# Optimization experiments

Measured on AMD Instinct MI355X. Metric: run time of the kernel, lower is better.

The kernel has to match this reference:

```python
import math
import jax, jax.numpy as jnp
import numpy as np

B, T, H = 4096, 49, 512

def setup_inputs() -> dict:
    key = jax.random.key(0)
    ks = jax.random.split(key, 13)
    sc = 1.0 / math.sqrt(H)
    return {
        "v": jax.random.normal(ks[0], (B, T, H), dtype=jnp.float32),
        "h": jax.random.normal(ks[1], (B, H), dtype=jnp.float32),
        "s": jax.random.normal(ks[2], (B, H), dtype=jnp.float32),
        "W_h": jax.random.normal(ks[3], (H, H), dtype=jnp.float32) * sc,
        "b_h": jax.random.normal(ks[4], (H,), dtype=jnp.float32) * sc,
        "W_v": jax.random.normal(ks[5], (H, H), dtype=jnp.float32) * sc,
        "b_v": jax.random.normal(ks[6], (H,), dtype=jnp.float32) * sc,
        "w_z": jax.random.normal(ks[7], (H,), dtype=jnp.float32) * sc,
        "b_z": jax.random.normal(ks[8], (), dtype=jnp.float32) * sc,
        "W_s": jax.random.normal(ks[9], (H, H), dtype=jnp.float32) * sc,
        "b_s": jax.random.normal(ks[10], (H,), dtype=jnp.float32) * sc,
        "w_beta": jax.random.normal(ks[11], (H,), dtype=jnp.float32) * sc,
        "b_beta": jax.random.normal(ks[12], (), dtype=jnp.float32) * sc,
    }

def reference(v, h, s, W_h, b_h, W_v, b_v, w_z, b_z, W_s, b_s, w_beta, b_beta):
    # eval mode: dropout is identity
    h_proj = h @ W_h + b_h                                  # [B, H]
    v_proj = jnp.einsum('bth,hk->btk', v, W_v) + b_v        # [B, T, H]
    z = jnp.tanh(h_proj[:, None, :] + v_proj)               # [B, T, H]
    z = jnp.einsum('bth,h->bt', z, w_z) + b_z               # [B, T]
    beta = jnp.tanh((s @ W_s + b_s + h_proj) * math.sqrt(0.5))  # [B, H]
    beta = (beta @ w_beta + b_beta)[:, None]                # [B, 1]
    a = jax.nn.softmax(jnp.concatenate([z, beta], axis=1), axis=1)  # [B, T+1]
    v_ext = jnp.concatenate([v, s[:, None, :]], axis=1)     # [B, T+1, H]
    c = jnp.einsum('bt,bth->bh', a, v_ext)                  # [B, H]
    return c
```

## Files before the change

kernel.cpp:

```cpp
#include <hip/hip_runtime.h>
#include <stdint.h>

#define B_ 4096
#define T_ 49
#define H_ 512
#define BT_ (B_*T_)
#define BB 16

typedef __bf16 bf16x8 __attribute__((ext_vector_type(8)));
typedef float  f32x4  __attribute__((ext_vector_type(4)));
typedef unsigned short ushort_;

__device__ __forceinline__ ushort_ f2bf(float f){
  unsigned int u = __float_as_uint(f);
  u += 0x7fffu + ((u >> 16) & 1u);
  return (ushort_)(u >> 16);
}

__device__ __forceinline__ float fast_tanh(float x){
  float e = __expf(2.0f * x);
  return 1.0f - 2.0f * __builtin_amdgcn_rcpf(e + 1.0f);
}

__global__ __launch_bounds__(256) void k_pack(const float* __restrict__ W,
                                              ushort_* __restrict__ pack){
  int idx = blockIdx.x * 256 + threadIdx.x;
  int lane = idx & 63;
  int gt   = (idx >> 6) & 31;
  int kk   = idx >> 11;
  int col  = gt*16 + (lane & 15);
  int k0   = kk*32 + (lane >> 4)*8;
  ushort4 lo, hi;
  lo.x = f2bf(W[(k0+0)*H_ + col]);
  lo.y = f2bf(W[(k0+1)*H_ + col]);
  lo.z = f2bf(W[(k0+2)*H_ + col]);
  lo.w = f2bf(W[(k0+3)*H_ + col]);
  hi.x = f2bf(W[(k0+4)*H_ + col]);
  hi.y = f2bf(W[(k0+5)*H_ + col]);
  hi.z = f2bf(W[(k0+6)*H_ + col]);
  hi.w = f2bf(W[(k0+7)*H_ + col]);
  ushort4* dst = (ushort4*)pack;
  dst[idx*2]   = lo;
  dst[idx*2+1] = hi;
}

__global__ __launch_bounds__(256) void k_proj2(
    const float* __restrict__ h, const float* __restrict__ s,
    const ushort_* __restrict__ whp, const ushort_* __restrict__ wsp,
    const float* __restrict__ bh, const float* __restrict__ bs,
    const float* __restrict__ bv, const float* __restrict__ wbeta,
    const float* __restrict__ bbeta_p,
    float* __restrict__ hpb, float* __restrict__ beta)
{
  __shared__ __align__(16) ushort_ hl[16*H_];
  __shared__ __align__(16) ushort_ sl[16*H_];
  __shared__ float zwp[4][16];
  const int tid = threadIdx.x;
  const int w = tid >> 6, lane = tid & 63;
  const int l15 = lane & 15, l4 = lane >> 4;
  const int b0 = blockIdx.x * 16;

  {
    const int r = tid >> 4;
    const float4* hsrc = (const float4*)(h + (size_t)(b0+r)*H_);
    const float4* ssrc = (const float4*)(s + (size_t)(b0+r)*H_);
    #pragma unroll
    for(int p=0;p<8;p++){
      int q  = (tid & 15) + p*16;
      int k0 = q*4;
      float4 fh = hsrc[q];
      float4 fs = ssrc[q];
      int idx = (k0>>5)*512 + ((((k0&31)>>3)<<4) + r)*8 + (k0&7);
      ushort4 uh; uh.x=f2bf(fh.x); uh.y=f2bf(fh.y); uh.z=f2bf(fh.z); uh.w=f2bf(fh.w);
      ushort4 us; us.x=f2bf(fs.x); us.y=f2bf(fs.y); us.z=f2bf(fs.z); us.w=f2bf(fs.w);
      *(ushort4*)&hl[idx] = uh;
      *(ushort4*)&sl[idx] = us;
    }
  }
  __syncthreads();

  const bf16x8* __restrict__ bph = (const bf16x8*)whp;
  const bf16x8* __restrict__ bps = (const bf16x8*)wsp;
  const int bbase = w*512 + lane;

  f32x4 acch[8], accs[8];
  #pragma unroll
  for(int ni=0;ni<8;ni++){ acch[ni]=(f32x4){0,0,0,0}; accs[ni]=(f32x4){0,0,0,0}; }

  #pragma unroll 2
  for(int kk=0;kk<16;kk++){
    bf16x8 ah = *(const bf16x8*)&hl[kk*512 + lane*8];
    bf16x8 as2 = *(const bf16x8*)&sl[kk*512 + lane*8];
    #pragma unroll
    for(int ni=0;ni<8;ni++){
      acch[ni] = __builtin_amdgcn_mfma_f32_16x16x32_bf16(ah,  bph[kk*2048 + bbase + ni*64], acch[ni], 0,0,0);
      accs[ni] = __builtin_amdgcn_mfma_f32_16x16x32_bf16(as2, bps[kk*2048 + bbase + ni*64], accs[ni], 0,0,0);
    }
  }

  float bhv[8], bsv[8], bvv[8], wbv[8];
  #pragma unroll
  for(int ni=0;ni<8;ni++){
    int col = w*128 + ni*16 + l15;
    bhv[ni] = bh[col]; bsv[ni] = bs[col]; bvv[ni] = bv[col]; wbv[ni] = wbeta[col];
  }
  float btsum[4];
  #pragma unroll
  for(int rr=0;rr<4;rr++){
    int row = l4*4 + rr;
    float bsum = 0.f;
    #pragma unroll
    for(int ni=0;ni<8;ni++){
      int col = w*128 + ni*16 + l15;
      float hp = acch[ni][rr] + bhv[ni];
      hpb[(size_t)(b0+row)*H_ + col] = hp + bvv[ni];
      float bt = fast_tanh((accs[ni][rr] + bsv[ni] + hp) * 0.70710678118654752f);
      bsum = fmaf(bt, wbv[ni], bsum);
    }
    btsum[rr] = bsum;
  }
  #pragma unroll
  for(int rr=0;rr<4;rr++){
    btsum[rr] += __shfl_xor(btsum[rr], 1);
    btsum[rr] += __shfl_xor(btsum[rr], 2);
    btsum[rr] += __shfl_xor(btsum[rr], 4);
    btsum[rr] += __shfl_xor(btsum[rr], 8);
    if(l15 == 0) zwp[w][l4*4+rr] = btsum[rr];
  }
  __syncthreads();
  if(tid < 16)
    beta[b0+tid] = zwp[0][tid] + zwp[1][tid] + zwp[2][tid] + zwp[3][tid] + bbeta_p[0];
}

__global__ __launch_bounds__(256, 2) void k_fused(
    const float* __restrict__ v, const ushort_* __restrict__ bpack,
    const float* __restrict__ hpb, const float* __restrict__ wz,
    const float* __restrict__ bz_p, const float* __restrict__ beta,
    const float* __restrict__ s, float* __restrict__ out)
{
  __shared__ __align__(16) ushort_ Av[49*512];
  __shared__ float zw[4][64];
  __shared__ float a_s[64];
  const int tid = threadIdx.x;
  const int w = tid >> 6, lane = tid & 63;
  const int l15 = lane & 15, l4 = lane >> 4;
  const int b = blockIdx.x;

  const f32x4* __restrict__ vsrc = (const f32x4*)(v + (size_t)b * T_ * H_);
  const bf16x8* __restrict__ bp = (const bf16x8*)bpack;
  const int bbase = w*512 + lane;

  const int srow = tid >> 4, c4 = tid & 15;
  const int slot = ((c4 >> 1) ^ (srow & 7));
  const int wsub = ((c4 & 1) << 3);

  {
    f32x4 nf0 = __builtin_nontemporal_load(vsrc + (srow      )*128 + c4);
    f32x4 nf1 = __builtin_nontemporal_load(vsrc + (srow + 16 )*128 + c4);
    f32x4 nf2 = __builtin_nontemporal_load(vsrc + (srow + 32 )*128 + c4);
    f32x4 nf3;
    if(tid < 16) nf3 = __builtin_nontemporal_load(vsrc + 48*128 + c4);
    ushort4 u;
    u.x=f2bf(nf0[0]); u.y=f2bf(nf0[1]); u.z=f2bf(nf0[2]); u.w=f2bf(nf0[3]);
    *(ushort4*)((char*)Av + (srow   )*1024 + (slot<<4) + wsub) = u;
    u.x=f2bf(nf1[0]); u.y=f2bf(nf1[1]); u.z=f2bf(nf1[2]); u.w=f2bf(nf1[3]);
    *(ushort4*)((char*)Av + (srow+16)*1024 + (slot<<4) + wsub) = u;
    u.x=f2bf(nf2[0]); u.y=f2bf(nf2[1]); u.z=f2bf(nf2[2]); u.w=f2bf(nf2[3]);
    *(ushort4*)((char*)Av + (srow+32)*1024 + (slot<<4) + wsub) = u;
    if(tid < 16){
      u.x=f2bf(nf3[0]); u.y=f2bf(nf3[1]); u.z=f2bf(nf3[2]); u.w=f2bf(nf3[3]);
      *(ushort4*)((char*)Av + 48*1024 + (slot<<4) + wsub) = u;
    }
  }

  f32x4 acc[4][8];
  #pragma unroll
  for(int mi=0;mi<4;mi++)
    #pragma unroll
    for(int ni=0;ni<8;ni++) acc[mi][ni] = (f32x4){0.f,0.f,0.f,0.f};

  __syncthreads();

  #pragma unroll 1
  for(int c=0;c<8;c++){
    bf16x8 b0[8], b1[8];
    #pragma unroll
    for(int ni=0;ni<8;ni++) b0[ni] = bp[(2*c  )*2048 + bbase + ni*64];
    #pragma unroll
    for(int ni=0;ni<8;ni++) b1[ni] = bp[(2*c+1)*2048 + bbase + ni*64];
    f32x4 nf0, nf1, nf2, nf3;
    if(c < 7){
      nf0 = __builtin_nontemporal_load(vsrc + (srow      )*128 + (c+1)*16 + c4);
      nf1 = __builtin_nontemporal_load(vsrc + (srow + 16 )*128 + (c+1)*16 + c4);
      nf2 = __builtin_nontemporal_load(vsrc + (srow + 32 )*128 + (c+1)*16 + c4);
      if(tid < 16) nf3 = __builtin_nontemporal_load(vsrc + 48*128 + (c+1)*16 + c4);
    }
    bf16x8 af[4];
    #pragma unroll
    for(int mi=0;mi<4;mi++){
      int row = (mi < 3) ? (mi*16 + l15) : 48;
      int g   = ((2*c)*4 + l4) ^ (row & 7);
      af[mi] = *(const bf16x8*)((const char*)Av + row*1024 + (g<<4));
    }
    #pragma unroll
    for(int mi=0;mi<4;mi++)
      #pragma unroll
      for(int ni=0;ni<8;ni++)
        acc[mi][ni] = __builtin_amdgcn_mfma_f32_16x16x32_bf16(af[mi], b0[ni], acc[mi][ni], 0,0,0);
    #pragma unroll
    for(int mi=0;mi<4;mi++){
      int row = (mi < 3) ? (mi*16 + l15) : 48;
      int g   = ((2*c+1)*4 + l4) ^ (row & 7);
      af[mi] = *(const bf16x8*)((const char*)Av + row*1024 + (g<<4));
    }
    #pragma unroll
    for(int mi=0;mi<4;mi++)
      #pragma unroll
      for(int ni=0;ni<8;ni++)
        acc[mi][ni] = __builtin_amdgcn_mfma_f32_16x16x32_bf16(af[mi], b1[ni], acc[mi][ni], 0,0,0);
    if(c < 7){
      const int cb = (c+1)*128;
      ushort4 u;
      u.x=f2bf(nf0[0]); u.y=f2bf(nf0[1]); u.z=f2bf(nf0[2]); u.w=f2bf(nf0[3]);
      *(ushort4*)((char*)Av + (srow   )*1024 + cb + (slot<<4) + wsub) = u;
      u.x=f2bf(nf1[0]); u.y=f2bf(nf1[1]); u.z=f2bf(nf1[2]); u.w=f2bf(nf1[3]);
      *(ushort4*)((char*)Av + (srow+16)*1024 + cb + (slot<<4) + wsub) = u;
      u.x=f2bf(nf2[0]); u.y=f2bf(nf2[1]); u.z=f2bf(nf2[2]); u.w=f2bf(nf2[3]);
      *(ushort4*)((char*)Av + (srow+32)*1024 + cb + (slot<<4) + wsub) = u;
      if(tid < 16){
        u.x=f2bf(nf3[0]); u.y=f2bf(nf3[1]); u.z=f2bf(nf3[2]); u.w=f2bf(nf3[3]);
        *(ushort4*)((char*)Av + 48*1024 + cb + (slot<<4) + wsub) = u;
      }
    }
    __syncthreads();
  }

  float wzv[8], hp0[8];
  #pragma unroll
  for(int ni=0;ni<8;ni++){
    int col = w*128 + ni*16 + l15;
    wzv[ni] = wz[col];
    hp0[ni] = hpb[(size_t)b*H_ + col];
  }
  float zp[16];
  #pragma unroll
  for(int mi=0;mi<4;mi++){
    #pragma unroll
    for(int r=0;r<4;r++){
      float az = 0.f;
      #pragma unroll
      for(int ni=0;ni<8;ni++)
        az = fmaf(fast_tanh(acc[mi][ni][r] + hp0[ni]), wzv[ni], az);
      zp[mi*4+r] = az;
    }
  }
  #pragma unroll
  for(int i=0;i<16;i++){
    zp[i] += __shfl_xor(zp[i], 1);
    zp[i] += __shfl_xor(zp[i], 2);
    zp[i] += __shfl_xor(zp[i], 4);
    zp[i] += __shfl_xor(zp[i], 8);
  }
  if(l15 == 0){
    #pragma unroll
    for(int mi=0;mi<4;mi++)
      #pragma unroll
      for(int r=0;r<4;r++)
        zw[w][mi*16 + l4*4 + r] = zp[mi*4+r];
  }
  __syncthreads();

  if(tid < 64){
    float zv;
    if(tid < T_)       zv = zw[0][tid] + zw[1][tid] + zw[2][tid] + zw[3][tid] + bz_p[0];
    else if(tid == T_) zv = beta[b];
    else               zv = -3.0e38f;
    float m = zv;
    #pragma unroll
    for(int off=32;off>=1;off>>=1) m = fmaxf(m, __shfl_xor(m, off));
    float e = (tid <= T_) ? __expf(zv - m) : 0.f;
    float ssum = e;
    #pragma unroll
    for(int off=32;off>=1;off>>=1) ssum += __shfl_xor(ssum, off);
    a_s[tid] = e * __builtin_amdgcn_rcpf(ssum);
  }
  __syncthreads();

  const int n0 = tid * 2;
  float ax = 0.f, ay = 0.f;
  #pragma unroll 7
  for(int t=0;t<T_;t++){
    float at = a_s[t];
    unsigned int u = *(const unsigned int*)((const char*)Av + t*1024
                       + ((((n0>>3) ^ (t&7)))<<4) + ((n0&7)<<1));
    float x = __uint_as_float((u & 0xFFFFu) << 16);
    float y = __uint_as_float(u & 0xFFFF0000u);
    ax = fmaf(at, x, ax);
    ay = fmaf(at, y, ay);
  }
  float a49 = a_s[T_];
  float2 sv = ((const float2*)(s + (size_t)b*H_))[tid];
  ax = fmaf(a49, sv.x, ax);
  ay = fmaf(a49, sv.y, ay);
  float2 res; res.x = ax; res.y = ay;
  ((float2*)(out + (size_t)b*H_))[tid] = res;
}

extern "C" void kernel_launch(void* const* d_in, const int* in_sizes, int n_in,
                              void* d_out, int out_size, void* d_ws, size_t ws_size,
                              hipStream_t stream)
{
  const float* v   = (const float*)d_in[0];
  const float* h   = (const float*)d_in[1];
  const float* s   = (const float*)d_in[2];
  const float* Wh  = (const float*)d_in[3];
  const float* bh  = (const float*)d_in[4];
  const float* Wv  = (const float*)d_in[5];
  const float* bv  = (const float*)d_in[6];
  const float* wz  = (const float*)d_in[7];
  const float* bz  = (const float*)d_in[8];
  const float* Ws  = (const float*)d_in[9];
  const float* bs  = (const float*)d_in[10];
  const float* wb  = (const float*)d_in[11];
  const float* bbet= (const float*)d_in[12];
  float* out = (float*)d_out;

  float* hpb  = (float*)d_ws;
  float* beta = hpb + (size_t)B_*H_;
  ushort_* bpack = (ushort_*)(beta + B_);
  ushort_* whp   = bpack + (size_t)H_*H_;
  ushort_* wsp   = whp   + (size_t)H_*H_;

  k_pack <<<128, 256, 0, stream>>>(Wv, bpack);
  k_pack <<<128, 256, 0, stream>>>(Wh, whp);
  k_pack <<<128, 256, 0, stream>>>(Ws, wsp);
  k_proj2<<<B_/16, 256, 0, stream>>>(h, s, whp, wsp, bh, bs, bv, wb, bbet, hpb, beta);
  k_fused<<<B_, 256, 0, stream>>>(v, bpack, hpb, wz, bz, beta, s, out);
}
```

Baseline: 217.2 us.

## Split fused GEMM into two N-halves to cut registers and raise occupancy

The fused kernel now computes the v·W_v projection in two passes over column halves, each with a 4x4 accumulator tile instead of 4x8. This roughly halves accumulator registers so the launch bound can be raised from 2 to 3 blocks per CU, which should better hide the latency of the global v loads. It also double-buffers the W fragment loads across k-steps and raises wave priority around the MFMA blocks. In exchange, the staged bf16 v tile is read from LDS twice and the tanh/w_z reduction runs twice, accumulating into shared memory.

```diff
diff --git a/kernel.cpp b/kernel.cpp
--- a/kernel.cpp
+++ b/kernel.cpp
@@ -132,7 +132,7 @@
     beta[b0+tid] = zwp[0][tid] + zwp[1][tid] + zwp[2][tid] + zwp[3][tid] + bbeta_p[0];
 }
 
-__global__ __launch_bounds__(256, 2) void k_fused(
+__global__ __launch_bounds__(256, 3) void k_fused(
     const float* __restrict__ v, const ushort_* __restrict__ bpack,
     const float* __restrict__ hpb, const float* __restrict__ wz,
     const float* __restrict__ bz_p, const float* __restrict__ beta,
@@ -148,7 +148,7 @@
 
   const f32x4* __restrict__ vsrc = (const f32x4*)(v + (size_t)b * T_ * H_);
   const bf16x8* __restrict__ bp = (const bf16x8*)bpack;
-  const int bbase = w*512 + lane;
+  const int bbase = w*256 + lane;
 
   const int srow = tid >> 4, c4 = tid & 15;
   const int slot = ((c4 >> 1) ^ (srow & 7));
@@ -173,21 +173,21 @@
     }
   }
 
-  f32x4 acc[4][8];
+  f32x4 acc[4][4];
   #pragma unroll
   for(int mi=0;mi<4;mi++)
     #pragma unroll
-    for(int ni=0;ni<8;ni++) acc[mi][ni] = (f32x4){0.f,0.f,0.f,0.f};
-
+    for(int ni=0;ni<4;ni++) acc[mi][ni] = (f32x4){0.f,0.f,0.f,0.f};
+
+  bf16x8 ba[4], bb[4];
+  #pragma unroll
+  for(int ni=0;ni<4;ni++) ba[ni] = bp[bbase + ni*64];
   __syncthreads();
 
   #pragma unroll 1
   for(int c=0;c<8;c++){
-    bf16x8 b0[8], b1[8];
-    #pragma unroll
-    for(int ni=0;ni<8;ni++) b0[ni] = bp[(2*c  )*2048 + bbase + ni*64];
-    #pragma unroll
-    for(int ni=0;ni<8;ni++) b1[ni] = bp[(2*c+1)*2048 + bbase + ni*64];
+    #pragma unroll
+    for(int ni=0;ni<4;ni++) bb[ni] = bp[(2*c+1)*2048 + bbase + ni*64];
     f32x4 nf0, nf1, nf2, nf3;
     if(c < 7){
       nf0 = __builtin_nontemporal_load(vsrc + (srow      )*128 + (c+1)*16 + c4);
@@ -202,22 +202,30 @@
       int g   = ((2*c)*4 + l4) ^ (row & 7);
       af[mi] = *(const bf16x8*)((const char*)Av + row*1024 + (g<<4));
     }
-    #pragma unroll
-    for(int mi=0;mi<4;mi++)
-      #pragma unroll
-      for(int ni=0;ni<8;ni++)
-        acc[mi][ni] = __builtin_amdgcn_mfma_f32_16x16x32_bf16(af[mi], b0[ni], acc[mi][ni], 0,0,0);
+    __builtin_amdgcn_s_setprio(1);
+    #pragma unroll
+    for(int mi=0;mi<4;mi++)
+      #pragma unroll
+      for(int ni=0;ni<4;ni++)
+        acc[mi][ni] = __builtin_amdgcn_mfma_f32_16x16x32_bf16(af[mi], ba[ni], acc[mi][ni], 0,0,0);
+    __builtin_amdgcn_s_setprio(0);
+    if(c < 7){
+      #pragma unroll
+      for(int ni=0;ni<4;ni++) ba[ni] = bp[(2*c+2)*2048 + bbase + ni*64];
+    }
     #pragma unroll
     for(int mi=0;mi<4;mi++){
       int row = (mi < 3) ? (mi*16 + l15) : 48;
       int g   = ((2*c+1)*4 + l4) ^ (row & 7);
       af[mi] = *(const bf16x8*)((const char*)Av + row*1024 + (g<<4));
     }
-    #pragma unroll
-    for(int mi=0;mi<4;mi++)
-      #pragma unroll
-      for(int ni=0;ni<8;ni++)
-        acc[mi][ni] = __builtin_amdgcn_mfma_f32_16x16x32_bf16(af[mi], b1[ni], acc[mi][ni], 0,0,0);
+    __builtin_amdgcn_s_setprio(1);
+    #pragma unroll
+    for(int mi=0;mi<4;mi++)
+      #pragma unroll
+      for(int ni=0;ni<4;ni++)
+        acc[mi][ni] = __builtin_amdgcn_mfma_f32_16x16x32_bf16(af[mi], bb[ni], acc[mi][ni], 0,0,0);
+    __builtin_amdgcn_s_setprio(0);
     if(c < 7){
       const int cb = (c+1)*128;
       ushort4 u;
@@ -231,42 +239,123 @@
         u.x=f2bf(nf3[0]); u.y=f2bf(nf3[1]); u.z=f2bf(nf3[2]); u.w=f2bf(nf3[3]);
         *(ushort4*)((char*)Av + 48*1024 + cb + (slot<<4) + wsub) = u;
       }
-    }
-    __syncthreads();
-  }
-
-  float wzv[8], hp0[8];
-  #pragma unroll
-  for(int ni=0;ni<8;ni++){
-    int col = w*128 + ni*16 + l15;
-    wzv[ni] = wz[col];
-    hp0[ni] = hpb[(size_t)b*H_ + col];
-  }
-  float zp[16];
-  #pragma unroll
-  for(int mi=0;mi<4;mi++){
-    #pragma unroll
-    for(int r=0;r<4;r++){
-      float az = 0.f;
-      #pragma unroll
-      for(int ni=0;ni<8;ni++)
-        az = fmaf(fast_tanh(acc[mi][ni][r] + hp0[ni]), wzv[ni], az);
-      zp[mi*4+r] = az;
-    }
-  }
-  #pragma unroll
-  for(int i=0;i<16;i++){
-    zp[i] += __shfl_xor(zp[i], 1);
-    zp[i] += __shfl_xor(zp[i], 2);
-    zp[i] += __shfl_xor(zp[i], 4);
-    zp[i] += __shfl_xor(zp[i], 8);
-  }
-  if(l15 == 0){
-    #pragma unroll
-    for(int mi=0;mi<4;mi++)
-      #pragma unroll
-      for(int r=0;r<4;r++)
-        zw[w][mi*16 + l4*4 + r] = zp[mi*4+r];
+      __syncthreads();
+    }
+  }
+
+  {
+    float wzv[4], hp0[4];
+    #pragma unroll
+    for(int ni=0;ni<4;ni++){
+      int col = w*64 + ni*16 + l15;
+      wzv[ni] = wz[col];
+      hp0[ni] = hpb[(size_t)b*H_ + col];
+    }
+    float zp[16];
+    #pragma unroll
+    for(int mi=0;mi<4;mi++)
+      #pragma unroll
+      for(int r=0;r<4;r++){
+        float az = 0.f;
+        #pragma unroll
+        for(int ni=0;ni<4;ni++)
+          az = fmaf(fast_tanh(acc[mi][ni][r] + hp0[ni]), wzv[ni], az);
+        zp[mi*4+r] = az;
+      }
+    #pragma unroll
+    for(int i=0;i<16;i++){
+      zp[i] += __shfl_xor(zp[i], 1);
+      zp[i] += __shfl_xor(zp[i], 2);
+      zp[i] += __shfl_xor(zp[i], 4);
+      zp[i] += __shfl_xor(zp[i], 8);
+    }
+    if(l15 == 0){
+      #pragma unroll
+      for(int mi=0;mi<4;mi++)
+        #pragma unroll
+        for(int r=0;r<4;r++)
+          zw[w][mi*16 + l4*4 + r] = zp[mi*4+r];
+    }
+  }
+
+  #pragma unroll
+  for(int mi=0;mi<4;mi++)
+    #pragma unroll
+    for(int ni=0;ni<4;ni++) acc[mi][ni] = (f32x4){0.f,0.f,0.f,0.f};
+
+  #pragma unroll
+  for(int ni=0;ni<4;ni++) ba[ni] = bp[1024 + bbase + ni*64];
+
+  #pragma unroll 1
+  for(int k2=0;k2<8;k2++){
+    #pragma unroll
+    for(int ni=0;ni<4;ni++) bb[ni] = bp[(2*k2+1)*2048 + 1024 + bbase + ni*64];
+    bf16x8 af[4];
+    #pragma unroll
+    for(int mi=0;mi<4;mi++){
+      int row = (mi < 3) ? (mi*16 + l15) : 48;
+      int g   = ((2*k2)*4 + l4) ^ (row & 7);
+      af[mi] = *(const bf16x8*)((const char*)Av + row*1024 + (g<<4));
+    }
+    __builtin_amdgcn_s_setprio(1);
+    #pragma unroll
+    for(int mi=0;mi<4;mi++)
+      #pragma unroll
+      for(int ni=0;ni<4;ni++)
+        acc[mi][ni] = __builtin_amdgcn_mfma_f32_16x16x32_bf16(af[mi], ba[ni], acc[mi][ni], 0,0,0);
+    __builtin_amdgcn_s_setprio(0);
+    if(k2 < 7){
+      #pragma unroll
+      for(int ni=0;ni<4;ni++) ba[ni] = bp[(2*k2+2)*2048 + 1024 + bbase + ni*64];
+    }
+    #pragma unroll
+    for(int mi=0;mi<4;mi++){
+      int row = (mi < 3) ? (mi*16 + l15) : 48;
+      int g   = ((2*k2+1)*4 + l4) ^ (row & 7);
+      af[mi] = *(const bf16x8*)((const char*)Av + row*1024 + (g<<4));
+    }
+    __builtin_amdgcn_s_setprio(1);
+    #pragma unroll
+    for(int mi=0;mi<4;mi++)
+      #pragma unroll
+      for(int ni=0;ni<4;ni++)
+        acc[mi][ni] = __builtin_amdgcn_mfma_f32_16x16x32_bf16(af[mi], bb[ni], acc[mi][ni], 0,0,0);
+    __builtin_amdgcn_s_setprio(0);
+  }
+
+  {
+    float wzv[4], hp0[4];
+    #pragma unroll
+    for(int ni=0;ni<4;ni++){
+      int col = 256 + w*64 + ni*16 + l15;
+      wzv[ni] = wz[col];
+      hp0[ni] = hpb[(size_t)b*H_ + col];
+    }
+    float zp[16];
+    #pragma unroll
+    for(int mi=0;mi<4;mi++)
+      #pragma unroll
+      for(int r=0;r<4;r++){
+        float az = 0.f;
+        #pragma unroll
+        for(int ni=0;ni<4;ni++)
+          az = fmaf(fast_tanh(acc[mi][ni][r] + hp0[ni]), wzv[ni], az);
+        zp[mi*4+r] = az;
+      }
+    #pragma unroll
+    for(int i=0;i<16;i++){
+      zp[i] += __shfl_xor(zp[i], 1);
+      zp[i] += __shfl_xor(zp[i], 2);
+      zp[i] += __shfl_xor(zp[i], 4);
+      zp[i] += __shfl_xor(zp[i], 8);
+    }
+    if(l15 == 0){
+      #pragma unroll
+      for(int mi=0;mi<4;mi++)
+        #pragma unroll
+        for(int r=0;r<4;r++)
+          zw[w][mi*16 + l4*4 + r] += zp[mi*4+r];
+    }
   }
   __syncthreads();
 
```

Measured after the change: 213.5 us. Within noise of the previous version (-1.7%).

## Split output columns into two passes to halve accumulator registers, deepen v prefetch

Applied to the files above, without the earlier changes.

Each wave now covers 64 output columns per pass instead of 128. The kernel runs two passes over the bf16 v tile held in LDS: the first pass overlaps with streaming v in from global memory, and the second reuses the full tile already in LDS. The accumulator drops from 32 to 16 f32x4 registers, and v loads are double-buffered two chunks ahead, with s_setprio raised around the MFMA groups. The aim is to free registers and hide global latency, at the cost of a second sweep of A-fragment LDS reads and a second tanh reduction pass.

```diff
diff --git a/kernel.cpp b/kernel.cpp
--- a/kernel.cpp
+++ b/kernel.cpp
@@ -148,125 +148,175 @@
 
   const f32x4* __restrict__ vsrc = (const f32x4*)(v + (size_t)b * T_ * H_);
   const bf16x8* __restrict__ bp = (const bf16x8*)bpack;
-  const int bbase = w*512 + lane;
+  const int bbase = w*256 + lane;
 
   const int srow = tid >> 4, c4 = tid & 15;
   const int slot = ((c4 >> 1) ^ (srow & 7));
   const int wsub = ((c4 & 1) << 3);
+  const bool r48 = (tid < 16);
+
+#define VLOAD(N0,N1,N2,N3, CH) { \
+    N0 = __builtin_nontemporal_load(vsrc + (srow     )*128 + (CH)*16 + c4); \
+    N1 = __builtin_nontemporal_load(vsrc + (srow + 16)*128 + (CH)*16 + c4); \
+    N2 = __builtin_nontemporal_load(vsrc + (srow + 32)*128 + (CH)*16 + c4); \
+    if(r48) N3 = __builtin_nontemporal_load(vsrc + 48*128 + (CH)*16 + c4); }
+
+#define SWRITE(N0,N1,N2,N3, CH) { \
+    const int cb_ = (CH)*128; ushort4 u_; \
+    u_.x=f2bf(N0[0]); u_.y=f2bf(N0[1]); u_.z=f2bf(N0[2]); u_.w=f2bf(N0[3]); \
+    *(ushort4*)((char*)Av + (srow   )*1024 + cb_ + (slot<<4) + wsub) = u_; \
+    u_.x=f2bf(N1[0]); u_.y=f2bf(N1[1]); u_.z=f2bf(N1[2]); u_.w=f2bf(N1[3]); \
+    *(ushort4*)((char*)Av + (srow+16)*1024 + cb_ + (slot<<4) + wsub) = u_; \
+    u_.x=f2bf(N2[0]); u_.y=f2bf(N2[1]); u_.z=f2bf(N2[2]); u_.w=f2bf(N2[3]); \
+    *(ushort4*)((char*)Av + (srow+32)*1024 + cb_ + (slot<<4) + wsub) = u_; \
+    if(r48){ \
+      u_.x=f2bf(N3[0]); u_.y=f2bf(N3[1]); u_.z=f2bf(N3[2]); u_.w=f2bf(N3[3]); \
+      *(ushort4*)((char*)Av + 48*1024 + cb_ + (slot<<4) + wsub) = u_; } }
+
+#define AFRAG(af, KS) { \
+    _Pragma("unroll") \
+    for(int mi=0;mi<4;mi++){ \
+      int row_ = (mi < 3) ? (mi*16 + l15) : 48; \
+      int g_   = ((KS)*4 + l4) ^ (row_ & 7); \
+      af[mi] = *(const bf16x8*)((const char*)Av + row_*1024 + (g_<<4)); } }
+
+#define MFMA16(af, bfr) { \
+    __builtin_amdgcn_s_setprio(1); \
+    _Pragma("unroll") \
+    for(int mi=0;mi<4;mi++) \
+      _Pragma("unroll") \
+      for(int ni=0;ni<4;ni++) \
+        acc[mi][ni] = __builtin_amdgcn_mfma_f32_16x16x32_bf16(af[mi], bfr[ni], acc[mi][ni], 0,0,0); \
+    __builtin_amdgcn_s_setprio(0); }
+
+  f32x4 A0,A1,A2,A3, B0,B1,B2,B3;
+  f32x4 acc[4][4];
+  #pragma unroll
+  for(int mi=0;mi<4;mi++)
+    #pragma unroll
+    for(int ni=0;ni<4;ni++) acc[mi][ni] = (f32x4){0.f,0.f,0.f,0.f};
+
+  VLOAD(A0,A1,A2,A3, 0)
+  SWRITE(A0,A1,A2,A3, 0)
+  VLOAD(A0,A1,A2,A3, 1)
+  VLOAD(B0,B1,B2,B3, 2)
+
+  bf16x8 ba[4], bb[4], af[4];
+  #pragma unroll
+  for(int ni=0;ni<4;ni++) ba[ni] = bp[bbase + ni*64];
+  __syncthreads();
+
+#define BODY(C, W0,W1,W2,W3) { \
+    _Pragma("unroll") \
+    for(int ni=0;ni<4;ni++) bb[ni] = bp[(2*(C)+1)*2048 + bbase + ni*64]; \
+    AFRAG(af, 2*(C)) \
+    MFMA16(af, ba) \
+    if((C) < 7){ SWRITE(W0,W1,W2,W3, (C)+1) } \
+    if((C) < 5){ VLOAD(W0,W1,W2,W3, (C)+3) } \
+    if((C) < 7){ \
+      _Pragma("unroll") \
+      for(int ni=0;ni<4;ni++) ba[ni] = bp[(2*(C)+2)*2048 + bbase + ni*64]; } \
+    AFRAG(af, 2*(C)+1) \
+    MFMA16(af, bb) \
+    __syncthreads(); }
+
+  #pragma unroll 1
+  for(int cc=0; cc<4; cc++){
+    const int c0 = 2*cc;
+    BODY(c0,   A0,A1,A2,A3)
+    BODY(c0+1, B0,B1,B2,B3)
+  }
 
   {
-    f32x4 nf0 = __builtin_nontemporal_load(vsrc + (srow      )*128 + c4);
-    f32x4 nf1 = __builtin_nontemporal_load(vsrc + (srow + 16 )*128 + c4);
-    f32x4 nf2 = __builtin_nontemporal_load(vsrc + (srow + 32 )*128 + c4);
-    f32x4 nf3;
-    if(tid < 16) nf3 = __builtin_nontemporal_load(vsrc + 48*128 + c4);
-    ushort4 u;
-    u.x=f2bf(nf0[0]); u.y=f2bf(nf0[1]); u.z=f2bf(nf0[2]); u.w=f2bf(nf0[3]);
-    *(ushort4*)((char*)Av + (srow   )*1024 + (slot<<4) + wsub) = u;
-    u.x=f2bf(nf1[0]); u.y=f2bf(nf1[1]); u.z=f2bf(nf1[2]); u.w=f2bf(nf1[3]);
-    *(ushort4*)((char*)Av + (srow+16)*1024 + (slot<<4) + wsub) = u;
-    u.x=f2bf(nf2[0]); u.y=f2bf(nf2[1]); u.z=f2bf(nf2[2]); u.w=f2bf(nf2[3]);
-    *(ushort4*)((char*)Av + (srow+32)*1024 + (slot<<4) + wsub) = u;
-    if(tid < 16){
-      u.x=f2bf(nf3[0]); u.y=f2bf(nf3[1]); u.z=f2bf(nf3[2]); u.w=f2bf(nf3[3]);
-      *(ushort4*)((char*)Av + 48*1024 + (slot<<4) + wsub) = u;
-    }
-  }
-
-  f32x4 acc[4][8];
+    float wzv[4], hp0[4];
+    #pragma unroll
+    for(int ni=0;ni<4;ni++){
+      int col = w*64 + ni*16 + l15;
+      wzv[ni] = wz[col];
+      hp0[ni] = hpb[(size_t)b*H_ + col];
+    }
+    float zp[16];
+    #pragma unroll
+    for(int mi=0;mi<4;mi++)
+      #pragma unroll
+      for(int r=0;r<4;r++){
+        float az = 0.f;
+        #pragma unroll
+        for(int ni=0;ni<4;ni++)
+          az = fmaf(fast_tanh(acc[mi][ni][r] + hp0[ni]), wzv[ni], az);
+        zp[mi*4+r] = az;
+      }
+    #pragma unroll
+    for(int i=0;i<16;i++){
+      zp[i] += __shfl_xor(zp[i], 1);
+      zp[i] += __shfl_xor(zp[i], 2);
+      zp[i] += __shfl_xor(zp[i], 4);
+      zp[i] += __shfl_xor(zp[i], 8);
+    }
+    if(l15 == 0){
+      #pragma unroll
+      for(int mi=0;mi<4;mi++)
+        #pragma unroll
+        for(int r=0;r<4;r++)
+          zw[w][mi*16 + l4*4 + r] = zp[mi*4+r];
+    }
+  }
+
   #pragma unroll
   for(int mi=0;mi<4;mi++)
     #pragma unroll
-    for(int ni=0;ni<8;ni++) acc[mi][ni] = (f32x4){0.f,0.f,0.f,0.f};
-
-  __syncthreads();
+    for(int ni=0;ni<4;ni++) acc[mi][ni] = (f32x4){0.f,0.f,0.f,0.f};
+
+  #pragma unroll
+  for(int ni=0;ni<4;ni++) ba[ni] = bp[1024 + bbase + ni*64];
 
   #pragma unroll 1
-  for(int c=0;c<8;c++){
-    bf16x8 b0[8], b1[8];
-    #pragma unroll
-    for(int ni=0;ni<8;ni++) b0[ni] = bp[(2*c  )*2048 + bbase + ni*64];
-    #pragma unroll
-    for(int ni=0;ni<8;ni++) b1[ni] = bp[(2*c+1)*2048 + bbase + ni*64];
-    f32x4 nf0, nf1, nf2, nf3;
-    if(c < 7){
-      nf0 = __builtin_nontemporal_load(vsrc + (srow      )*128 + (c+1)*16 + c4);
-      nf1 = __builtin_nontemporal_load(vsrc + (srow + 16 )*128 + (c+1)*16 + c4);
-      nf2 = __builtin_nontemporal_load(vsrc + (srow + 32 )*128 + (c+1)*16 + c4);
-      if(tid < 16) nf3 = __builtin_nontemporal_load(vsrc + 48*128 + (c+1)*16 + c4);
-    }
-    bf16x8 af[4];
-    #pragma unroll
-    for(int mi=0;mi<4;mi++){
-      int row = (mi < 3) ? (mi*16 + l15) : 48;
-      int g   = ((2*c)*4 + l4) ^ (row & 7);
-      af[mi] = *(const bf16x8*)((const char*)Av + row*1024 + (g<<4));
-    }
+  for(int k2=0;k2<8;k2++){
+    #pragma unroll
+    for(int ni=0;ni<4;ni++) bb[ni] = bp[(2*k2+1)*2048 + 1024 + bbase + ni*64];
+    AFRAG(af, 2*k2)
+    MFMA16(af, ba)
+    if(k2 < 7){
+      #pragma unroll
+      for(int ni=0;ni<4;ni++) ba[ni] = bp[(2*k2+2)*2048 + 1024 + bbase + ni*64];
+    }
+    AFRAG(af, 2*k2+1)
+    MFMA16(af, bb)
+  }
+
+  {
+    float wzv[4], hp0[4];
+    #pragma unroll
+    for(int ni=0;ni<4;ni++){
+      int col = 256 + w*64 + ni*16 + l15;
+      wzv[ni] = wz[col];
+      hp0[ni] = hpb[(size_t)b*H_ + col];
+    }
+    float zp[16];
     #pragma unroll
     for(int mi=0;mi<4;mi++)
       #pragma unroll
-      for(int ni=0;ni<8;ni++)
-        acc[mi][ni] = __builtin_amdgcn_mfma_f32_16x16x32_bf16(af[mi], b0[ni], acc[mi][ni], 0,0,0);
-    #pragma unroll
-    for(int mi=0;mi<4;mi++){
-      int row = (mi < 3) ? (mi*16 + l15) : 48;
-      int g   = ((2*c+1)*4 + l4) ^ (row & 7);
-      af[mi] = *(const bf16x8*)((const char*)Av + row*1024 + (g<<4));
-    }
-    #pragma unroll
-    for(int mi=0;mi<4;mi++)
-      #pragma unroll
-      for(int ni=0;ni<8;ni++)
-        acc[mi][ni] = __builtin_amdgcn_mfma_f32_16x16x32_bf16(af[mi], b1[ni], acc[mi][ni], 0,0,0);
-    if(c < 7){
-      const int cb = (c+1)*128;
-      ushort4 u;
-      u.x=f2bf(nf0[0]); u.y=f2bf(nf0[1]); u.z=f2bf(nf0[2]); u.w=f2bf(nf0[3]);
-      *(ushort4*)((char*)Av + (srow   )*1024 + cb + (slot<<4) + wsub) = u;
-      u.x=f2bf(nf1[0]); u.y=f2bf(nf1[1]); u.z=f2bf(nf1[2]); u.w=f2bf(nf1[3]);
-      *(ushort4*)((char*)Av + (srow+16)*1024 + cb + (slot<<4) + wsub) = u;
-      u.x=f2bf(nf2[0]); u.y=f2bf(nf2[1]); u.z=f2bf(nf2[2]); u.w=f2bf(nf2[3]);
-      *(ushort4*)((char*)Av + (srow+32)*1024 + cb + (slot<<4) + wsub) = u;
-      if(tid < 16){
-        u.x=f2bf(nf3[0]); u.y=f2bf(nf3[1]); u.z=f2bf(nf3[2]); u.w=f2bf(nf3[3]);
-        *(ushort4*)((char*)Av + 48*1024 + cb + (slot<<4) + wsub) = u;
+      for(int r=0;r<4;r++){
+        float az = 0.f;
+        #pragma unroll
+        for(int ni=0;ni<4;ni++)
+          az = fmaf(fast_tanh(acc[mi][ni][r] + hp0[ni]), wzv[ni], az);
+        zp[mi*4+r] = az;
       }
-    }
-    __syncthreads();
-  }
-
-  float wzv[8], hp0[8];
-  #pragma unroll
-  for(int ni=0;ni<8;ni++){
-    int col = w*128 + ni*16 + l15;
-    wzv[ni] = wz[col];
-    hp0[ni] = hpb[(size_t)b*H_ + col];
-  }
-  float zp[16];
-  #pragma unroll
-  for(int mi=0;mi<4;mi++){
-    #pragma unroll
-    for(int r=0;r<4;r++){
-      float az = 0.f;
-      #pragma unroll
-      for(int ni=0;ni<8;ni++)
-        az = fmaf(fast_tanh(acc[mi][ni][r] + hp0[ni]), wzv[ni], az);
-      zp[mi*4+r] = az;
-    }
-  }
-  #pragma unroll
-  for(int i=0;i<16;i++){
-    zp[i] += __shfl_xor(zp[i], 1);
-    zp[i] += __shfl_xor(zp[i], 2);
-    zp[i] += __shfl_xor(zp[i], 4);
-    zp[i] += __shfl_xor(zp[i], 8);
-  }
-  if(l15 == 0){
-    #pragma unroll
-    for(int mi=0;mi<4;mi++)
-      #pragma unroll
-      for(int r=0;r<4;r++)
-        zw[w][mi*16 + l4*4 + r] = zp[mi*4+r];
+    #pragma unroll
+    for(int i=0;i<16;i++){
+      zp[i] += __shfl_xor(zp[i], 1);
+      zp[i] += __shfl_xor(zp[i], 2);
+      zp[i] += __shfl_xor(zp[i], 4);
+      zp[i] += __shfl_xor(zp[i], 8);
+    }
+    if(l15 == 0){
+      #pragma unroll
+      for(int mi=0;mi<4;mi++)
+        #pragma unroll
+        for(int r=0;r<4;r++)
+          zw[w][mi*16 + l4*4 + r] += zp[mi*4+r];
+    }
   }
   __syncthreads();
 
```

Measured after the change: 239.0 us. 10.0% more time.

## Persist fused kernel over 16 batches with double-buffered v staging

Applied to the files above, without the earlier changes.

The fused attention kernel becomes persistent: 256 blocks of 512 threads each loop over 16 batch rows. Each block double-buffers the bf16 copy of v in LDS, so loads of the next batch overlap the MFMA work on the current one. The B-fragment loads use a 3-deep register ring and MFMA issue is raised in priority with s_setprio. The risks are lower occupancy, since LDS doubles to about 98KB per block and only 256 blocks are launched, and more barriers per batch.

```diff
diff --git a/kernel.cpp b/kernel.cpp
--- a/kernel.cpp
+++ b/kernel.cpp
@@ -16,7 +16,9 @@
   u += 0x7fffu + ((u >> 16) & 1u);
   return (ushort_)(u >> 16);
 }
-
+__device__ __forceinline__ float bf2f(ushort_ u){
+  return __uint_as_float(((unsigned int)u) << 16);
+}
 __device__ __forceinline__ float fast_tanh(float x){
   float e = __expf(2.0f * x);
   return 1.0f - 2.0f * __builtin_amdgcn_rcpf(e + 1.0f);
@@ -132,178 +134,196 @@
     beta[b0+tid] = zwp[0][tid] + zwp[1][tid] + zwp[2][tid] + zwp[3][tid] + bbeta_p[0];
 }
 
-__global__ __launch_bounds__(256, 2) void k_fused(
+__global__ __launch_bounds__(512, 2) void k_fused(
     const float* __restrict__ v, const ushort_* __restrict__ bpack,
     const float* __restrict__ hpb, const float* __restrict__ wz,
     const float* __restrict__ bz_p, const float* __restrict__ beta,
     const float* __restrict__ s, float* __restrict__ out)
 {
-  __shared__ __align__(16) ushort_ Av[49*512];
-  __shared__ float zw[4][64];
+  __shared__ __align__(16) ushort_ Av[2*T_*H_];
+  __shared__ float zw[8][64];
   __shared__ float a_s[64];
   const int tid = threadIdx.x;
   const int w = tid >> 6, lane = tid & 63;
   const int l15 = lane & 15, l4 = lane >> 4;
-  const int b = blockIdx.x;
-
-  const f32x4* __restrict__ vsrc = (const f32x4*)(v + (size_t)b * T_ * H_);
+  const int blk = blockIdx.x;
+  const bool t128 = (tid < 128);
+
   const bf16x8* __restrict__ bp = (const bf16x8*)bpack;
-  const int bbase = w*512 + lane;
-
-  const int srow = tid >> 4, c4 = tid & 15;
-  const int slot = ((c4 >> 1) ^ (srow & 7));
-  const int wsub = ((c4 & 1) << 3);
+  const int bbase = w*256 + lane;
+
+  float wzv[4];
+  #pragma unroll
+  for(int ni=0;ni<4;ni++) wzv[ni] = wz[w*64 + ni*16 + l15];
+  const float bzv = bz_p[0];
+
+#define SIDX(J, ROW, C4, VI, WB) \
+    { int flat_ = (J < 12) ? (tid + (J)*512) : (6144 + tid); \
+      ROW = flat_ >> 7; C4 = flat_ & 127; \
+      VI = ROW*128 + C4; \
+      WB = ROW*1024 + ((((C4>>1) ^ (ROW&7)))<<4) + ((C4&1)<<3); }
+
+#define STAGE_ISSUE(SR, VS) { \
+    _Pragma("unroll") \
+    for(int j=0;j<12;j++){ int r_,c_,vi_,wb_; SIDX(j, r_,c_,vi_,wb_) \
+      SR[j] = __builtin_nontemporal_load((VS) + vi_); } \
+    if(t128){ int r_,c_,vi_,wb_; SIDX(12, r_,c_,vi_,wb_) \
+      SR[12] = __builtin_nontemporal_load((VS) + vi_); } }
+
+#define STAGE_WRITE(SR, DSTC) { \
+    _Pragma("unroll") \
+    for(int j=0;j<12;j++){ int r_,c_,vi_,wb_; SIDX(j, r_,c_,vi_,wb_) \
+      ushort4 u_; u_.x=f2bf(SR[j][0]); u_.y=f2bf(SR[j][1]); \
+      u_.z=f2bf(SR[j][2]); u_.w=f2bf(SR[j][3]); \
+      *(ushort4*)((DSTC) + wb_) = u_; } \
+    if(t128){ int r_,c_,vi_,wb_; SIDX(12, r_,c_,vi_,wb_) \
+      ushort4 u_; u_.x=f2bf(SR[12][0]); u_.y=f2bf(SR[12][1]); \
+      u_.z=f2bf(SR[12][2]); u_.w=f2bf(SR[12][3]); \
+      *(ushort4*)((DSTC) + wb_) = u_; } }
 
   {
-    f32x4 nf0 = __builtin_nontemporal_load(vsrc + (srow      )*128 + c4);
-    f32x4 nf1 = __builtin_nontemporal_load(vsrc + (srow + 16 )*128 + c4);
-    f32x4 nf2 = __builtin_nontemporal_load(vsrc + (srow + 32 )*128 + c4);
-    f32x4 nf3;
-    if(tid < 16) nf3 = __builtin_nontemporal_load(vsrc + 48*128 + c4);
-    ushort4 u;
-    u.x=f2bf(nf0[0]); u.y=f2bf(nf0[1]); u.z=f2bf(nf0[2]); u.w=f2bf(nf0[3]);
-    *(ushort4*)((char*)Av + (srow   )*1024 + (slot<<4) + wsub) = u;
-    u.x=f2bf(nf1[0]); u.y=f2bf(nf1[1]); u.z=f2bf(nf1[2]); u.w=f2bf(nf1[3]);
-    *(ushort4*)((char*)Av + (srow+16)*1024 + (slot<<4) + wsub) = u;
-    u.x=f2bf(nf2[0]); u.y=f2bf(nf2[1]); u.z=f2bf(nf2[2]); u.w=f2bf(nf2[3]);
-    *(ushort4*)((char*)Av + (srow+32)*1024 + (slot<<4) + wsub) = u;
-    if(tid < 16){
-      u.x=f2bf(nf3[0]); u.y=f2bf(nf3[1]); u.z=f2bf(nf3[2]); u.w=f2bf(nf3[3]);
-      *(ushort4*)((char*)Av + 48*1024 + (slot<<4) + wsub) = u;
-    }
-  }
-
-  f32x4 acc[4][8];
-  #pragma unroll
-  for(int mi=0;mi<4;mi++)
-    #pragma unroll
-    for(int ni=0;ni<8;ni++) acc[mi][ni] = (f32x4){0.f,0.f,0.f,0.f};
-
+    const f32x4* vs = (const f32x4*)(v + (size_t)(blk*16)*T_*H_);
+    f32x4 sr[13];
+    STAGE_ISSUE(sr, vs)
+    STAGE_WRITE(sr, (char*)Av)
+  }
   __syncthreads();
 
   #pragma unroll 1
-  for(int c=0;c<8;c++){
-    bf16x8 b0[8], b1[8];
-    #pragma unroll
-    for(int ni=0;ni<8;ni++) b0[ni] = bp[(2*c  )*2048 + bbase + ni*64];
-    #pragma unroll
-    for(int ni=0;ni<8;ni++) b1[ni] = bp[(2*c+1)*2048 + bbase + ni*64];
-    f32x4 nf0, nf1, nf2, nf3;
-    if(c < 7){
-      nf0 = __builtin_nontemporal_load(vsrc + (srow      )*128 + (c+1)*16 + c4);
-      nf1 = __builtin_nontemporal_load(vsrc + (srow + 16 )*128 + (c+1)*16 + c4);
-      nf2 = __builtin_nontemporal_load(vsrc + (srow + 32 )*128 + (c+1)*16 + c4);
-      if(tid < 16) nf3 = __builtin_nontemporal_load(vsrc + 48*128 + (c+1)*16 + c4);
-    }
-    bf16x8 af[4];
+  for(int bi=0; bi<16; bi++){
+    const int b = blk*16 + bi;
+    const char* curc = (const char*)Av + (bi&1)*(T_*H_*2);
+    char* nxtc = (char*)Av + ((bi+1)&1)*(T_*H_*2);
+
+    f32x4 acc[4][4];
+    #pragma unroll
+    for(int mi=0;mi<4;mi++)
+      #pragma unroll
+      for(int ni=0;ni<4;ni++) acc[mi][ni] = (f32x4){0.f,0.f,0.f,0.f};
+
+    bf16x8 bfr[3][4];
+    #pragma unroll
+    for(int p=0;p<3;p++)
+      #pragma unroll
+      for(int ni=0;ni<4;ni++) bfr[p][ni] = bp[p*2048 + bbase + ni*64];
+
+    bf16x8 af2[2][4];
     #pragma unroll
     for(int mi=0;mi<4;mi++){
-      int row = (mi < 3) ? (mi*16 + l15) : 48;
-      int g   = ((2*c)*4 + l4) ^ (row & 7);
-      af[mi] = *(const bf16x8*)((const char*)Av + row*1024 + (g<<4));
-    }
-    #pragma unroll
-    for(int mi=0;mi<4;mi++)
-      #pragma unroll
-      for(int ni=0;ni<8;ni++)
-        acc[mi][ni] = __builtin_amdgcn_mfma_f32_16x16x32_bf16(af[mi], b0[ni], acc[mi][ni], 0,0,0);
-    #pragma unroll
-    for(int mi=0;mi<4;mi++){
-      int row = (mi < 3) ? (mi*16 + l15) : 48;
-      int g   = ((2*c+1)*4 + l4) ^ (row & 7);
-      af[mi] = *(const bf16x8*)((const char*)Av + row*1024 + (g<<4));
-    }
-    #pragma unroll
-    for(int mi=0;mi<4;mi++)
-      #pragma unroll
-      for(int ni=0;ni<8;ni++)
-        acc[mi][ni] = __builtin_amdgcn_mfma_f32_16x16x32_bf16(af[mi], b1[ni], acc[mi][ni], 0,0,0);
-    if(c < 7){
-      const int cb = (c+1)*128;
-      ushort4 u;
-      u.x=f2bf(nf0[0]); u.y=f2bf(nf0[1]); u.z=f2bf(nf0[2]); u.w=f2bf(nf0[3]);
-      *(ushort4*)((char*)Av + (srow   )*1024 + cb + (slot<<4) + wsub) = u;
-      u.x=f2bf(nf1[0]); u.y=f2bf(nf1[1]); u.z=f2bf(nf1[2]); u.w=f2bf(nf1[3]);
-      *(ushort4*)((char*)Av + (srow+16)*1024 + cb + (slot<<4) + wsub) = u;
-      u.x=f2bf(nf2[0]); u.y=f2bf(nf2[1]); u.z=f2bf(nf2[2]); u.w=f2bf(nf2[3]);
-      *(ushort4*)((char*)Av + (srow+32)*1024 + cb + (slot<<4) + wsub) = u;
-      if(tid < 16){
-        u.x=f2bf(nf3[0]); u.y=f2bf(nf3[1]); u.z=f2bf(nf3[2]); u.w=f2bf(nf3[3]);
-        *(ushort4*)((char*)Av + 48*1024 + cb + (slot<<4) + wsub) = u;
+      int row = (mi<3) ? (mi*16 + l15) : 48;
+      int g   = (l4) ^ (row & 7);
+      af2[0][mi] = *(const bf16x8*)(curc + row*1024 + (g<<4));
+    }
+
+    float hpv[4];
+    #pragma unroll
+    for(int ni=0;ni<4;ni++) hpv[ni] = hpb[(size_t)b*H_ + w*64 + ni*16 + l15];
+    float btv = beta[b];
+
+    f32x4 sr[13];
+    if(bi < 15){
+      const f32x4* vs = (const f32x4*)(v + (size_t)(b+1)*T_*H_);
+      STAGE_ISSUE(sr, vs)
+    }
+
+    #pragma unroll
+    for(int kk=0; kk<16; kk++){
+      if(kk < 15){
+        #pragma unroll
+        for(int mi=0;mi<4;mi++){
+          int row = (mi<3) ? (mi*16 + l15) : 48;
+          int g   = ((kk+1)*4 + l4) ^ (row & 7);
+          af2[(kk+1)&1][mi] = *(const bf16x8*)(curc + row*1024 + (g<<4));
+        }
+      }
+      __builtin_amdgcn_s_setprio(1);
+      #pragma unroll
+      for(int mi=0;mi<4;mi++)
+        #pragma unroll
+        for(int ni=0;ni<4;ni++)
+          acc[mi][ni] = __builtin_amdgcn_mfma_f32_16x16x32_bf16(
+              af2[kk&1][mi], bfr[kk%3][ni], acc[mi][ni], 0,0,0);
+      __builtin_amdgcn_s_setprio(0);
+      if(kk < 13){
+        #pragma unroll
+        for(int ni=0;ni<4;ni++) bfr[kk%3][ni] = bp[(kk+3)*2048 + bbase + ni*64];
+      }
+      if(kk == 3 && bi < 15){
+        STAGE_WRITE(sr, nxtc)
+      }
+    }
+
+    {
+      float zp[16];
+      #pragma unroll
+      for(int mi=0;mi<4;mi++)
+        #pragma unroll
+        for(int r=0;r<4;r++){
+          float az = 0.f;
+          #pragma unroll
+          for(int ni=0;ni<4;ni++)
+            az = fmaf(fast_tanh(acc[mi][ni][r] + hpv[ni]), wzv[ni], az);
+          zp[mi*4+r] = az;
+        }
+      #pragma unroll
+      for(int i=0;i<16;i++){
+        zp[i] += __shfl_xor(zp[i], 1);
+        zp[i] += __shfl_xor(zp[i], 2);
+        zp[i] += __shfl_xor(zp[i], 4);
+        zp[i] += __shfl_xor(zp[i], 8);
+      }
+      if(l15 == 0){
+        #pragma unroll
+        for(int mi=0;mi<4;mi++)
+          #pragma unroll
+          for(int r=0;r<4;r++)
+            zw[w][mi*16 + l4*4 + r] = zp[mi*4+r];
       }
     }
     __syncthreads();
-  }
-
-  float wzv[8], hp0[8];
-  #pragma unroll
-  for(int ni=0;ni<8;ni++){
-    int col = w*128 + ni*16 + l15;
-    wzv[ni] = wz[col];
-    hp0[ni] = hpb[(size_t)b*H_ + col];
-  }
-  float zp[16];
-  #pragma unroll
-  for(int mi=0;mi<4;mi++){
-    #pragma unroll
-    for(int r=0;r<4;r++){
-      float az = 0.f;
-      #pragma unroll
-      for(int ni=0;ni<8;ni++)
-        az = fmaf(fast_tanh(acc[mi][ni][r] + hp0[ni]), wzv[ni], az);
-      zp[mi*4+r] = az;
-    }
-  }
-  #pragma unroll
-  for(int i=0;i<16;i++){
-    zp[i] += __shfl_xor(zp[i], 1);
-    zp[i] += __shfl_xor(zp[i], 2);
-    zp[i] += __shfl_xor(zp[i], 4);
-    zp[i] += __shfl_xor(zp[i], 8);
-  }
-  if(l15 == 0){
-    #pragma unroll
-    for(int mi=0;mi<4;mi++)
-      #pragma unroll
-      for(int r=0;r<4;r++)
-        zw[w][mi*16 + l4*4 + r] = zp[mi*4+r];
-  }
-  __syncthreads();
-
-  if(tid < 64){
-    float zv;
-    if(tid < T_)       zv = zw[0][tid] + zw[1][tid] + zw[2][tid] + zw[3][tid] + bz_p[0];
-    else if(tid == T_) zv = beta[b];
-    else               zv = -3.0e38f;
-    float m = zv;
-    #pragma unroll
-    for(int off=32;off>=1;off>>=1) m = fmaxf(m, __shfl_xor(m, off));
-    float e = (tid <= T_) ? __expf(zv - m) : 0.f;
-    float ssum = e;
-    #pragma unroll
-    for(int off=32;off>=1;off>>=1) ssum += __shfl_xor(ssum, off);
-    a_s[tid] = e * __builtin_amdgcn_rcpf(ssum);
-  }
-  __syncthreads();
-
-  const int n0 = tid * 2;
-  float ax = 0.f, ay = 0.f;
-  #pragma unroll 7
-  for(int t=0;t<T_;t++){
-    float at = a_s[t];
-    unsigned int u = *(const unsigned int*)((const char*)Av + t*1024
-                       + ((((n0>>3) ^ (t&7)))<<4) + ((n0&7)<<1));
-    float x = __uint_as_float((u & 0xFFFFu) << 16);
-    float y = __uint_as_float(u & 0xFFFF0000u);
-    ax = fmaf(at, x, ax);
-    ay = fmaf(at, y, ay);
-  }
-  float a49 = a_s[T_];
-  float2 sv = ((const float2*)(s + (size_t)b*H_))[tid];
-  ax = fmaf(a49, sv.x, ax);
-  ay = fmaf(a49, sv.y, ay);
-  float2 res; res.x = ax; res.y = ay;
-  ((float2*)(out + (size_t)b*H_))[tid] = res;
+
+    if(tid < 64){
+      float zv;
+      if(tid < T_)
+        zv = zw[0][tid]+zw[1][tid]+zw[2][tid]+zw[3][tid]
+           + zw[4][tid]+zw[5][tid]+zw[6][tid]+zw[7][tid] + bzv;
+      else if(tid == T_) zv = btv;
+      else               zv = -3.0e38f;
+      float m = zv;
+      #pragma unroll
+      for(int off=32;off>=1;off>>=1) m = fmaxf(m, __shfl_xor(m, off));
+      float e = (tid <= T_) ? __expf(zv - m) : 0.f;
+      float ssum = e;
+      #pragma unroll
+      for(int off=32;off>=1;off>>=1) ssum += __shfl_xor(ssum, off);
+      a_s[tid] = e * __builtin_amdgcn_rcpf(ssum);
+    }
+    __syncthreads();
+
+    if(t128){
+      const int c0 = tid * 4;
+      float ax0=0.f, ax1=0.f, ax2=0.f, ax3=0.f;
+      #pragma unroll 7
+      for(int t=0;t<T_;t++){
+        float at = a_s[t];
+        ushort4 uu = *(const ushort4*)(curc + t*1024
+                        + ((((c0>>3) ^ (t&7)))<<4) + ((c0&7)<<1));
+        ax0 = fmaf(at, bf2f(uu.x), ax0);
+        ax1 = fmaf(at, bf2f(uu.y), ax1);
+        ax2 = fmaf(at, bf2f(uu.z), ax2);
+        ax3 = fmaf(at, bf2f(uu.w), ax3);
+      }
+      float a49 = a_s[T_];
+      float4 sv = *(const float4*)(s + (size_t)b*H_ + c0);
+      ax0 = fmaf(a49, sv.x, ax0);
+      ax1 = fmaf(a49, sv.y, ax1);
+      ax2 = fmaf(a49, sv.z, ax2);
+      ax3 = fmaf(a49, sv.w, ax3);
+      float4 res; res.x=ax0; res.y=ax1; res.z=ax2; res.w=ax3;
+      *(float4*)(out + (size_t)b*H_ + c0) = res;
+    }
+    __syncthreads();
+  }
 }
 
 extern "C" void kernel_launch(void* const* d_in, const int* in_sizes, int n_in,
@@ -335,5 +355,5 @@
   k_pack <<<128, 256, 0, stream>>>(Wh, whp);
   k_pack <<<128, 256, 0, stream>>>(Ws, wsp);
   k_proj2<<<B_/16, 256, 0, stream>>>(h, s, whp, wsp, bh, bs, bv, wb, bbet, hpb, beta);
-  k_fused<<<B_, 256, 0, stream>>>(v, bpack, hpb, wz, bz, beta, s, out);
-}
+  k_fused<<<256, 512, 0, stream>>>(v, bpack, hpb, wz, bz, beta, s, out);
+}
```

Result: slower. 653.2 us (+200.7%).
